# Optimization experiments

Measured on AMD Instinct MI355X. Metric: run time of the kernel, lower is better.

Reference implementation:

```python
import jax, jax.numpy as jnp
import numpy as np
import math

B, LA, LB, D, H = 8, 2048, 2048, 512, 512

def setup_inputs() -> dict:
    key = jax.random.key(0)
    ks = jax.random.split(key, 6)
    return {
        "input_a": jax.random.normal(ks[0], (B, LA, D), dtype=jnp.float32),
        "input_b": jax.random.normal(ks[1], (B, LB, D), dtype=jnp.float32),
        "mask_a": jax.random.randint(ks[2], (B, LA), 0, 2, dtype=jnp.int32),
        "mask_b": jax.random.randint(ks[3], (B, LB), 0, 2, dtype=jnp.int32),
        "Wa": jax.random.normal(ks[4], (D, H), dtype=jnp.float32) * (1.0 / math.sqrt(D)),
        "ba": jnp.zeros((H,), dtype=jnp.float32),
        "Wb": jax.random.normal(ks[5], (D, H), dtype=jnp.float32) * (1.0 / math.sqrt(D)),
        "bb": jnp.zeros((H,), dtype=jnp.float32),
    }

def reference(input_a, input_b, mask_a, mask_b, Wa, ba, Wb, bb):
    scale = 1.0 / math.sqrt(D)  # math.sqrt(input_dim_a)
    mapped_a = input_a @ Wa + ba            # [B, La, H]
    mapped_b = input_b @ Wb + bb            # [B, Lb, H]
    # final_mask = (mask_a outer mask_b) == 0
    final_mask = (mask_a[:, :, None] * mask_b[:, None, :]) == 0  # [B, La, Lb]
    scores = jnp.einsum('bih,bjh->bij', mapped_a, mapped_b) * scale
    scores = jnp.where(final_mask, jnp.float32(-1e9), scores)
    # attentions_a = softmax over Lb; attentions_b^T = softmax over La axis
    att_a = jax.nn.softmax(scores, axis=-1)   # [B, La, Lb]
    att_bT = jax.nn.softmax(scores, axis=1)   # [B, La, Lb] (= attentions_b.transpose(1,2))
    output_a = jnp.einsum('bij,bjd->bid', att_bT, input_b)  # [B, La, D]
    output_b = jnp.einsum('bij,bid->bjd', att_a, input_a)   # [B, Lb, D]
    return (output_a + input_a, output_b + input_b)
```

## Files before the change

### kernel.cpp

```cpp
#include <hip/hip_runtime.h>
#include <hip/hip_bf16.h>

#define BATCH 8
#define LSEQ 2048
#define DDIM 512

using f32x4 = __attribute__((ext_vector_type(4))) float;
using s16x8 = __attribute__((ext_vector_type(8))) short;
using s16x4 = __attribute__((ext_vector_type(4))) short;

static __device__ __forceinline__ unsigned short f2b(float f) {
  __hip_bfloat16 h = __float2bfloat16(f);
  return __builtin_bit_cast(unsigned short, h);
}
static __device__ __forceinline__ float b2f(unsigned short u) {
  unsigned int v = ((unsigned int)u) << 16;
  return __builtin_bit_cast(float, v);
}

static __device__ __forceinline__ void gld16(const unsigned short* g, unsigned short* l) {
  __builtin_amdgcn_global_load_lds(
      (__attribute__((address_space(1))) void*)(g),
      (__attribute__((address_space(3))) void*)(l), 16, 0, 0);
}

__device__ __forceinline__ void mfma_kloop(
    const unsigned short* __restrict__ A, const unsigned short* __restrict__ Bt,
    int K, int lda, int ldb, unsigned short* sA, unsigned short* sB,
    int tid, f32x4 acc[4][4]) {
  const int wave = tid >> 6, lane = tid & 63;
  const int wm = (wave >> 1) * 64, wn = (wave & 1) * 64;
  const int lr = lane & 15, lq = lane >> 4;
  const int srow = tid >> 2;
  const int sk = (tid & 3) * 8;
  unsigned short* dA0 = sA + wave * 512;
  unsigned short* dA1 = sA + 2048 + wave * 512;
  unsigned short* dB0 = sB + wave * 512;
  unsigned short* dB1 = sB + 2048 + wave * 512;
  const unsigned short* pa0 = A + (size_t)srow * lda + sk;
  const unsigned short* pa1 = A + (size_t)(srow + 64) * lda + sk;
  const unsigned short* pb0 = Bt + (size_t)srow * ldb + sk;
  const unsigned short* pb1 = Bt + (size_t)(srow + 64) * ldb + sk;
  for (int k0 = 0; k0 < K; k0 += 32) {
    gld16(pa0 + k0, dA0);
    gld16(pa1 + k0, dA1);
    gld16(pb0 + k0, dB0);
    gld16(pb1 + k0, dB1);
    __syncthreads();
    s16x8 af[4], bf[4];
#pragma unroll
    for (int r = 0; r < 4; ++r)
      af[r] = *(const s16x8*)(sA + (wm + r * 16 + lr) * 32 + lq * 8);
#pragma unroll
    for (int c = 0; c < 4; ++c)
      bf[c] = *(const s16x8*)(sB + (wn + c * 16 + lr) * 32 + lq * 8);
#pragma unroll
    for (int r = 0; r < 4; ++r)
#pragma unroll
      for (int c = 0; c < 4; ++c)
        acc[r][c] = __builtin_amdgcn_mfma_f32_16x16x32_bf16(af[r], bf[c], acc[r][c], 0, 0, 0);
    __syncthreads();
  }
}

__global__ __launch_bounds__(256) void k_prep(const float* __restrict__ in_a,
                                              const float* __restrict__ in_b,
                                              const int* __restrict__ ma,
                                              const int* __restrict__ mb,
                                              unsigned short* __restrict__ oa,
                                              unsigned short* __restrict__ ob,
                                              float* __restrict__ Pa,
                                              float* __restrict__ Pb) {
  int z = blockIdx.z;
  const float* in = z ? in_b : in_a;
  const int* mask = z ? mb : ma;
  unsigned short* o16 = z ? ob : oa;
  float* partial = z ? Pb : Pa;
  int b = blockIdx.y;
  int l0 = blockIdx.x * 32;
  __shared__ int sm[32];
  if (threadIdx.x < 32) sm[threadIdx.x] = mask[b * LSEQ + l0 + threadIdx.x];
  __syncthreads();
  int d = threadIdx.x * 2;
  const float* base = in + ((size_t)b * LSEQ + l0) * DDIM + d;
  unsigned short* obase = o16 + ((size_t)b * LSEQ + l0) * DDIM + d;
  float ax = 0.f, ay = 0.f;
#pragma unroll 4
  for (int r = 0; r < 32; ++r) {
    float2 v = *(const float2*)(base + (size_t)r * DDIM);
    ushort2 u; u.x = f2b(v.x); u.y = f2b(v.y);
    *(ushort2*)(obase + (size_t)r * DDIM) = u;
    if (sm[r] == 0) { ax += v.x; ay += v.y; }
  }
  float2 o; o.x = ax; o.y = ay;
  *(float2*)(partial + ((size_t)(b * 64 + blockIdx.x)) * DDIM + d) = o;
}

__global__ __launch_bounds__(256) void k_p2(const float* __restrict__ Pa,
                                            const float* __restrict__ Pb,
                                            float* __restrict__ Ca,
                                            float* __restrict__ Cb) {
  int g = blockIdx.x;
  const float* src = (g < 8) ? Pa : Pb;
  float* dst = (g < 8) ? Ca : Cb;
  int b = g & 7;
  int d = threadIdx.x * 2;
  float ax = 0.f, ay = 0.f;
  for (int c = 0; c < 64; ++c) {
    float2 v = *(const float2*)(src + ((size_t)(b * 64 + c)) * DDIM + d);
    ax += v.x; ay += v.y;
  }
  dst[b * DDIM + d] = ax * (1.0f / LSEQ);
  dst[b * DDIM + d + 1] = ay * (1.0f / LSEQ);
}

__global__ __launch_bounds__(256) void k_transposeW(const float* __restrict__ Wa,
                                                    const float* __restrict__ Wb,
                                                    unsigned short* __restrict__ WaT,
                                                    unsigned short* __restrict__ WbT) {
  int gidx = blockIdx.x * 256 + threadIdx.x;
  const float* W = (gidx < 512 * 512) ? Wa : Wb;
  unsigned short* WT = (gidx < 512 * 512) ? WaT : WbT;
  int idx = gidx & (512 * 512 - 1);
  int h = idx >> 9, d = idx & 511;
  WT[idx] = f2b(W[d * DDIM + h]);
}

__global__ __launch_bounds__(256) void k_gemm_bias(const unsigned short* __restrict__ a16,
                                                   const unsigned short* __restrict__ b16,
                                                   const unsigned short* __restrict__ WaT,
                                                   const unsigned short* __restrict__ WbT,
                                                   const float* __restrict__ ba,
                                                   const float* __restrict__ bb,
                                                   unsigned short* __restrict__ mapa,
                                                   unsigned short* __restrict__ mapb) {
  int id = blockIdx.x;
  int g = id >> 5, rem = id & 31;
  int bn = (rem >> 3) * 128;
  int f = g * 8 + (rem & 7);
  int bm = (f & 127) * 128;
  int z = f >> 7;
  const unsigned short* A = z ? b16 : a16;
  const unsigned short* Bt = z ? WbT : WaT;
  const float* bias = z ? bb : ba;
  unsigned short* Cout = z ? mapb : mapa;
  __shared__ __align__(16) unsigned short sA[128 * 32], sB[128 * 32];
  f32x4 acc[4][4];
  f32x4 zero = {0.f, 0.f, 0.f, 0.f};
#pragma unroll
  for (int r = 0; r < 4; ++r)
#pragma unroll
    for (int c = 0; c < 4; ++c) acc[r][c] = zero;
  mfma_kloop(A + (size_t)bm * DDIM, Bt + (size_t)bn * DDIM, DDIM, DDIM, DDIM,
             sA, sB, threadIdx.x, acc);
  int wave = threadIdx.x >> 6, lane = threadIdx.x & 63;
  int wm = (wave >> 1) * 64, wn = (wave & 1) * 64, lr = lane & 15, lq = lane >> 4;
#pragma unroll
  for (int r = 0; r < 4; ++r)
#pragma unroll
    for (int c = 0; c < 4; ++c)
#pragma unroll
      for (int rr = 0; rr < 4; ++rr) {
        int row = bm + wm + r * 16 + lq * 4 + rr;
        int col = bn + wn + c * 16 + lr;
        Cout[(size_t)row * DDIM + col] = f2b(acc[r][c][rr] + bias[col]);
      }
}

__global__ __launch_bounds__(256) void k_scores(const unsigned short* __restrict__ mapa,
                                                const unsigned short* __restrict__ mapb,
                                                const int* __restrict__ mask_a,
                                                const int* __restrict__ mask_b,
                                                unsigned short* __restrict__ E,
                                                unsigned short* __restrict__ Et,
                                                float* __restrict__ Zrow,
                                                float* __restrict__ Zcol) {
  int id = blockIdx.x;
  int low = id & 7, rest = id >> 3;
  int sub = rest & 15, Ghi = rest >> 4;
  int G = Ghi * 8 + low;
  int b = G >> 4, super = G & 15;
  int bi = (((super >> 2) << 2) + (sub >> 2)) * 128;
  int bj = (((super & 3) << 2) + (sub & 3)) * 128;
  __shared__ __align__(16) unsigned short smem[16384];
  __shared__ int sMa[128], sMb[128];
  int tid = threadIdx.x;
  if (tid < 128)
    sMa[tid] = mask_a[b * LSEQ + bi + tid];
  else
    sMb[tid - 128] = mask_b[b * LSEQ + bj + tid - 128];
  f32x4 acc[4][4];
  f32x4 zero = {0.f, 0.f, 0.f, 0.f};
#pragma unroll
  for (int r = 0; r < 4; ++r)
#pragma unroll
    for (int c = 0; c < 4; ++c) acc[r][c] = zero;
  mfma_kloop(mapa + ((size_t)b * LSEQ + bi) * DDIM, mapb + ((size_t)b * LSEQ + bj) * DDIM,
             DDIM, DDIM, DDIM, smem, smem + 4096, tid, acc);
  const float scale = 0.044194173824159216f;
  int wave = tid >> 6, lane = tid & 63;
  int wm = (wave >> 1) * 64, wn = (wave & 1) * 64, lr = lane & 15, lq = lane >> 4;
  unsigned short* Eb = E + (size_t)b * LSEQ * LSEQ + (size_t)bi * LSEQ + bj;
  float colp[4] = {0.f, 0.f, 0.f, 0.f};
  float rowp[4][4];
#pragma unroll
  for (int r = 0; r < 4; ++r) {
#pragma unroll
    for (int rr = 0; rr < 4; ++rr) rowp[r][rr] = 0.f;
#pragma unroll
    for (int c = 0; c < 4; ++c) {
      int jl = wn + c * 16 + lr;
      int mb_ = sMb[jl];
      s16x4 t;
#pragma unroll
      for (int rr = 0; rr < 4; ++rr) {
        int il = wm + r * 16 + lq * 4 + rr;
        float e = (sMa[il] && mb_) ? __expf(acc[r][c][rr] * scale) : 0.f;
        rowp[r][rr] += e;
        colp[c] += e;
        unsigned short eb = f2b(e);
        t[rr] = (short)eb;
        Eb[(size_t)il * LSEQ + jl] = eb;
      }
      int il0 = wm + r * 16 + lq * 4;
      *(s16x4*)(smem + jl * 128 + (il0 ^ ((jl & 7) << 4))) = t;
    }
  }
#pragma unroll
  for (int r = 0; r < 4; ++r)
#pragma unroll
    for (int rr = 0; rr < 4; ++rr) {
      float v = rowp[r][rr];
      v += __shfl_xor(v, 1);
      v += __shfl_xor(v, 2);
      v += __shfl_xor(v, 4);
      v += __shfl_xor(v, 8);
      if (lr == 0) {
        int il = wm + r * 16 + lq * 4 + rr;
        atomicAdd(&Zrow[b * LSEQ + bi + il], v);
      }
    }
#pragma unroll
  for (int c = 0; c < 4; ++c) {
    float v = colp[c];
    v += __shfl_xor(v, 16);
    v += __shfl_xor(v, 32);
    if (lq == 0) atomicAdd(&Zcol[b * LSEQ + bj + wn + c * 16 + lr], v);
  }
  __syncthreads();
  unsigned short* EtB = Et + (size_t)b * LSEQ * LSEQ + (size_t)bj * LSEQ + bi;
#pragma unroll
  for (int p = 0; p < 8; ++p) {
    int idx = p * 256 + tid;
    int jlr = idx >> 4, chk = idx & 15;
    s16x8 v = *(const s16x8*)(smem + jlr * 128 + ((chk * 8) ^ ((jlr & 7) << 4)));
    *(s16x8*)(EtB + (size_t)jlr * LSEQ + chk * 8) = v;
  }
}

__global__ __launch_bounds__(256) void k_scaleT(const unsigned short* __restrict__ a16,
                                                const unsigned short* __restrict__ b16,
                                                const float* __restrict__ Zrow,
                                                const float* __restrict__ Zcol,
                                                unsigned short* __restrict__ atS,
                                                unsigned short* __restrict__ btS) {
  int zz = blockIdx.z;
  int b = zz & 7, sel = zz >> 3;
  const unsigned short* in = sel ? b16 : a16;
  const float* Z = sel ? Zcol : Zrow;
  unsigned short* out = sel ? btS : atS;
  int i0 = blockIdx.y * 64, d0 = blockIdx.x * 64;
  __shared__ unsigned short lt[64 * 65];
  __shared__ float zinv[64];
  if (threadIdx.x < 64) {
    float z = Z[b * LSEQ + i0 + threadIdx.x];
    zinv[threadIdx.x] = (z > 0.f) ? 1.f / z : 0.f;
  }
  __syncthreads();
  const unsigned short* ib = in + ((size_t)b * LSEQ + i0) * DDIM + d0;
#pragma unroll
  for (int p = 0; p < 16; ++p) {
    int idx = p * 256 + threadIdx.x;
    int dl = idx & 63, il = idx >> 6;
    lt[dl * 65 + il] = f2b(b2f(ib[(size_t)il * DDIM + dl]) * zinv[il]);
  }
  __syncthreads();
  unsigned short* ob = out + ((size_t)b * DDIM + d0) * LSEQ + i0;
#pragma unroll
  for (int p = 0; p < 16; ++p) {
    int idx = p * 256 + threadIdx.x;
    int il = idx & 63, dl = idx >> 6;
    ob[(size_t)dl * LSEQ + il] = lt[dl * 65 + il];
  }
}

__global__ __launch_bounds__(512, 2) void k_gemm_outs(
    const unsigned short* __restrict__ E, const unsigned short* __restrict__ Et,
    const unsigned short* __restrict__ btS, const unsigned short* __restrict__ atS,
    const unsigned short* __restrict__ a16, const unsigned short* __restrict__ b16,
    const float* __restrict__ Ca, const float* __restrict__ Cb,
    float* __restrict__ OutA, float* __restrict__ OutB) {
  int w = (blockIdx.x & 7) * 32 + (blockIdx.x >> 3);
  int mode = w >> 7;
  int r0 = w & 127;
  int b = r0 >> 4, tile = r0 & 15;
  int bm = (tile >> 1) * 256, bn = (tile & 1) * 256;
  const unsigned short* Aop = (mode ? Et : E) + (size_t)b * LSEQ * LSEQ + (size_t)bm * LSEQ;
  const unsigned short* Bop = (mode ? atS : btS) + (size_t)b * DDIM * LSEQ + (size_t)bn * LSEQ;
  const unsigned short* addin = mode ? b16 : a16;
  const float* Cvec = mode ? Ca : Cb;
  float* Out = mode ? OutB : OutA;

  __shared__ __align__(16) unsigned short sA[4 * 8192], sB[4 * 8192];
  const int tid = threadIdx.x;
  const int wave = tid >> 6, lane = tid & 63;
  const int wr = wave >> 2, wc = wave & 3;
  const int lr = lane & 15, lq = lane >> 4;

  const int srow = tid >> 2;
  const int kcsw = ((tid & 3) ^ (srow & 3)) * 8;
  const unsigned short* pa0 = Aop + (size_t)srow * LSEQ + kcsw;
  const unsigned short* pa1 = pa0 + (size_t)128 * LSEQ;
  const unsigned short* pb0 = Bop + (size_t)srow * LSEQ + kcsw;
  const unsigned short* pb1 = pb0 + (size_t)128 * LSEQ;
  unsigned short* dA = sA + wave * 512;
  unsigned short* dB = sB + wave * 512;

  int aoff[8], boff[4];
#pragma unroll
  for (int m = 0; m < 8; ++m)
    aoff[m] = (wr * 128 + m * 16 + lr) * 32 + (lq ^ (lr & 3)) * 8;
#pragma unroll
  for (int n = 0; n < 4; ++n)
    boff[n] = (wc * 64 + n * 16 + lr) * 32 + (lq ^ (lr & 3)) * 8;

  f32x4 acc[8][4];
  f32x4 zero = {0.f, 0.f, 0.f, 0.f};
#pragma unroll
  for (int m = 0; m < 8; ++m)
#pragma unroll
    for (int n = 0; n < 4; ++n) acc[m][n] = zero;

#define SGA(c) { const int sl_ = ((c) & 3) * 8192; \
  gld16(pa0 + (size_t)(c) * 32, dA + sl_); \
  gld16(pa1 + (size_t)(c) * 32, dA + sl_ + 4096); }
#define SGB(c) { const int sl_ = ((c) & 3) * 8192; \
  gld16(pb0 + (size_t)(c) * 32, dB + sl_); \
  gld16(pb1 + (size_t)(c) * 32, dB + sl_ + 4096); }

  SGA(0); SGB(0); SGA(1); SGB(1); SGA(2); SGB(2);
  asm volatile("s_waitcnt vmcnt(8)\ns_barrier" ::: "memory");

  for (int j = 0; j < 64; ++j) {
    const int sl = (j & 3) * 8192;
    s16x8 af[8];
#pragma unroll
    for (int m = 0; m < 8; ++m) af[m] = *(const s16x8*)(sA + sl + aoff[m]);
    s16x8 bf0 = *(const s16x8*)(sB + sl + boff[0]);
    s16x8 bf1 = *(const s16x8*)(sB + sl + boff[1]);
    if (j < 61) SGA(j + 3);
    __builtin_amdgcn_s_setprio(1);
#pragma unroll
    for (int m = 0; m < 8; ++m) {
      acc[m][0] = __builtin_amdgcn_mfma_f32_16x16x32_bf16(af[m], bf0, acc[m][0], 0, 0, 0);
      acc[m][1] = __builtin_amdgcn_mfma_f32_16x16x32_bf16(af[m], bf1, acc[m][1], 0, 0, 0);
    }
    __builtin_amdgcn_s_setprio(0);
    asm volatile("s_barrier" ::: "memory");
    s16x8 bf2 = *(const s16x8*)(sB + sl + boff[2]);
    s16x8 bf3 = *(const s16x8*)(sB + sl + boff[3]);
    if (j < 61) SGB(j + 3);
    __builtin_amdgcn_s_setprio(1);
#pragma unroll
    for (int m = 0; m < 8; ++m) {
      acc[m][2] = __builtin_amdgcn_mfma_f32_16x16x32_bf16(af[m], bf2, acc[m][2], 0, 0, 0);
      acc[m][3] = __builtin_amdgcn_mfma_f32_16x16x32_bf16(af[m], bf3, acc[m][3], 0, 0, 0);
    }
    __builtin_amdgcn_s_setprio(0);
    if (j < 61)
      asm volatile("s_waitcnt vmcnt(8)\ns_barrier" ::: "memory");
    else if (j == 61)
      asm volatile("s_waitcnt vmcnt(4)\ns_barrier" ::: "memory");
    else
      asm volatile("s_waitcnt vmcnt(0)\ns_barrier" ::: "memory");
  }
#undef SGA
#undef SGB

#pragma unroll
  for (int m = 0; m < 8; ++m)
#pragma unroll
    for (int n = 0; n < 4; ++n)
#pragma unroll
      for (int rr = 0; rr < 4; ++rr) {
        int row = bm + wr * 128 + m * 16 + lq * 4 + rr;
        int col = bn + wc * 64 + n * 16 + lr;
        size_t o = ((size_t)b * LSEQ + row) * DDIM + col;
        Out[o] = acc[m][n][rr] + b2f(addin[o]) + Cvec[b * DDIM + col];
      }
}

extern "C" void kernel_launch(void* const* d_in, const int* in_sizes, int n_in,
                              void* d_out, int out_size, void* d_ws, size_t ws_size,
                              hipStream_t stream) {
  (void)in_sizes; (void)n_in; (void)out_size; (void)ws_size;
  const float* in_a = (const float*)d_in[0];
  const float* in_b = (const float*)d_in[1];
  const int* ma = (const int*)d_in[2];
  const int* mb = (const int*)d_in[3];
  const float* Wa = (const float*)d_in[4];
  const float* ba = (const float*)d_in[5];
  const float* Wb = (const float*)d_in[6];
  const float* bb = (const float*)d_in[7];
  float* out = (float*)d_out;

  char* ws = (char*)d_ws;
  const size_t MB = 1ull << 20;
  unsigned short* a16 = (unsigned short*)(ws + 0 * MB);
  unsigned short* b16 = (unsigned short*)(ws + 16 * MB);
  unsigned short* WaT = (unsigned short*)(ws + 32 * MB);
  unsigned short* WbT = (unsigned short*)(ws + 32 * MB + 512 * 1024);
  unsigned short* mapa = (unsigned short*)(ws + 33 * MB);
  unsigned short* mapb = (unsigned short*)(ws + 49 * MB);
  unsigned short* E = (unsigned short*)(ws + 65 * MB);
  unsigned short* atS = (unsigned short*)(ws + 129 * MB);
  unsigned short* btS = (unsigned short*)(ws + 145 * MB);
  float* Zrow = (float*)(ws + 161 * MB);
  float* Zcol = (float*)(ws + 161 * MB + 65536);
  float* Ca = (float*)(ws + 161 * MB + 2 * 65536);
  float* Cb = (float*)(ws + 161 * MB + 2 * 65536 + 16384);
  float* Pa = (float*)(ws + 162 * MB);
  float* Pb = (float*)(ws + 163 * MB);
  unsigned short* Et = (unsigned short*)(ws + 164 * MB);

  hipMemsetAsync(Zrow, 0, 2 * 65536, stream);
  k_prep<<<dim3(64, 8, 2), 256, 0, stream>>>(in_a, in_b, ma, mb, a16, b16, Pa, Pb);
  k_transposeW<<<2048, 256, 0, stream>>>(Wa, Wb, WaT, WbT);
  k_p2<<<16, 256, 0, stream>>>(Pa, Pb, Ca, Cb);
  k_gemm_bias<<<1024, 256, 0, stream>>>(a16, b16, WaT, WbT, ba, bb, mapa, mapb);
  k_scores<<<2048, 256, 0, stream>>>(mapa, mapb, ma, mb, E, Et, Zrow, Zcol);
  k_scaleT<<<dim3(8, 32, 16), 256, 0, stream>>>(a16, b16, Zrow, Zcol, atS, btS);
  k_gemm_outs<<<256, 512, 0, stream>>>(E, Et, btS, atS, a16, b16, Ca, Cb,
                                       out, out + (size_t)BATCH * LSEQ * DDIM);
}
```

Measured before the change: 324.7 us.

## Enlarge score tiles to 256x256 with pipelined 4-stage direct-to-LDS loads

Rewrites the scores GEMM kernel to use 256x256 output tiles with 512 threads (8 waves) instead of 128x128 with 256 threads. The new version uses a custom 4-slot ring of global_load_lds prefetches with manual vmcnt waits, splits the B fragment loads between two MFMA phases, and raises wave priority around the MFMA blocks. Larger tiles cut redundant operand loads and quarter the number of blocks. In exchange it uses 128KB of LDS and 128 accumulator registers per lane, which limits occupancy, and 512 blocks may leave the CUs less evenly loaded.

```diff
diff --git a/kernel.cpp b/kernel.cpp
--- a/kernel.cpp
+++ b/kernel.cpp
@@ -167,93 +167,158 @@
       }
 }
 
-__global__ __launch_bounds__(256) void k_scores(const unsigned short* __restrict__ mapa,
-                                                const unsigned short* __restrict__ mapb,
-                                                const int* __restrict__ mask_a,
-                                                const int* __restrict__ mask_b,
-                                                unsigned short* __restrict__ E,
-                                                unsigned short* __restrict__ Et,
-                                                float* __restrict__ Zrow,
-                                                float* __restrict__ Zcol) {
-  int id = blockIdx.x;
-  int low = id & 7, rest = id >> 3;
-  int sub = rest & 15, Ghi = rest >> 4;
-  int G = Ghi * 8 + low;
-  int b = G >> 4, super = G & 15;
-  int bi = (((super >> 2) << 2) + (sub >> 2)) * 128;
-  int bj = (((super & 3) << 2) + (sub & 3)) * 128;
-  __shared__ __align__(16) unsigned short smem[16384];
-  __shared__ int sMa[128], sMb[128];
-  int tid = threadIdx.x;
-  if (tid < 128)
+__global__ __launch_bounds__(512, 2) void k_scores(
+    const unsigned short* __restrict__ mapa, const unsigned short* __restrict__ mapb,
+    const int* __restrict__ mask_a, const int* __restrict__ mask_b,
+    unsigned short* __restrict__ E, unsigned short* __restrict__ Et,
+    float* __restrict__ Zrow, float* __restrict__ Zcol) {
+  int w = (blockIdx.x & 7) * 64 + (blockIdx.x >> 3);
+  int b = w >> 6, t = w & 63;
+  int bi = (t >> 3) * 256, bj = (t & 7) * 256;
+  const unsigned short* Aop = mapa + ((size_t)b * LSEQ + bi) * DDIM;
+  const unsigned short* Bop = mapb + ((size_t)b * LSEQ + bj) * DDIM;
+
+  __shared__ __align__(16) unsigned short smem[65536];
+  unsigned short* sA = smem;
+  unsigned short* sB = smem + 32768;
+  __shared__ int sMa[256], sMb[256];
+
+  const int tid = threadIdx.x;
+  const int wave = tid >> 6, lane = tid & 63;
+  const int wr = wave >> 2, wc = wave & 3;
+  const int lr = lane & 15, lq = lane >> 4;
+
+  const int srow = tid >> 2;
+  const int kcsw = ((tid & 3) ^ (srow & 3)) * 8;
+  const unsigned short* pa0 = Aop + (size_t)srow * DDIM + kcsw;
+  const unsigned short* pa1 = pa0 + (size_t)128 * DDIM;
+  const unsigned short* pb0 = Bop + (size_t)srow * DDIM + kcsw;
+  const unsigned short* pb1 = pb0 + (size_t)128 * DDIM;
+  unsigned short* dA = sA + wave * 512;
+  unsigned short* dB = sB + wave * 512;
+
+  int aoff[8], boff[4];
+#pragma unroll
+  for (int m = 0; m < 8; ++m)
+    aoff[m] = (wr * 128 + m * 16 + lr) * 32 + (lq ^ (lr & 3)) * 8;
+#pragma unroll
+  for (int n = 0; n < 4; ++n)
+    boff[n] = (wc * 64 + n * 16 + lr) * 32 + (lq ^ (lr & 3)) * 8;
+
+  f32x4 acc[8][4];
+  f32x4 zero = {0.f, 0.f, 0.f, 0.f};
+#pragma unroll
+  for (int m = 0; m < 8; ++m)
+#pragma unroll
+    for (int n = 0; n < 4; ++n) acc[m][n] = zero;
+
+#define SGA(c) { const int sl_ = ((c) & 3) * 8192; \
+  gld16(pa0 + (size_t)(c) * 32, dA + sl_); \
+  gld16(pa1 + (size_t)(c) * 32, dA + sl_ + 4096); }
+#define SGB(c) { const int sl_ = ((c) & 3) * 8192; \
+  gld16(pb0 + (size_t)(c) * 32, dB + sl_); \
+  gld16(pb1 + (size_t)(c) * 32, dB + sl_ + 4096); }
+
+  SGA(0); SGB(0); SGA(1); SGB(1); SGA(2); SGB(2);
+  asm volatile("s_waitcnt vmcnt(8)\ns_barrier" ::: "memory");
+
+  for (int j = 0; j < 16; ++j) {
+    const int sl = (j & 3) * 8192;
+    s16x8 af[8];
+#pragma unroll
+    for (int m = 0; m < 8; ++m) af[m] = *(const s16x8*)(sA + sl + aoff[m]);
+    s16x8 bf0 = *(const s16x8*)(sB + sl + boff[0]);
+    s16x8 bf1 = *(const s16x8*)(sB + sl + boff[1]);
+    if (j < 13) SGA(j + 3);
+    __builtin_amdgcn_s_setprio(1);
+#pragma unroll
+    for (int m = 0; m < 8; ++m) {
+      acc[m][0] = __builtin_amdgcn_mfma_f32_16x16x32_bf16(af[m], bf0, acc[m][0], 0, 0, 0);
+      acc[m][1] = __builtin_amdgcn_mfma_f32_16x16x32_bf16(af[m], bf1, acc[m][1], 0, 0, 0);
+    }
+    __builtin_amdgcn_s_setprio(0);
+    asm volatile("s_barrier" ::: "memory");
+    s16x8 bf2 = *(const s16x8*)(sB + sl + boff[2]);
+    s16x8 bf3 = *(const s16x8*)(sB + sl + boff[3]);
+    if (j < 13) SGB(j + 3);
+    __builtin_amdgcn_s_setprio(1);
+#pragma unroll
+    for (int m = 0; m < 8; ++m) {
+      acc[m][2] = __builtin_amdgcn_mfma_f32_16x16x32_bf16(af[m], bf2, acc[m][2], 0, 0, 0);
+      acc[m][3] = __builtin_amdgcn_mfma_f32_16x16x32_bf16(af[m], bf3, acc[m][3], 0, 0, 0);
+    }
+    __builtin_amdgcn_s_setprio(0);
+    if (j < 13)
+      asm volatile("s_waitcnt vmcnt(8)\ns_barrier" ::: "memory");
+    else if (j == 13)
+      asm volatile("s_waitcnt vmcnt(4)\ns_barrier" ::: "memory");
+    else
+      asm volatile("s_waitcnt vmcnt(0)\ns_barrier" ::: "memory");
+  }
+#undef SGA
+#undef SGB
+
+  if (tid < 256)
     sMa[tid] = mask_a[b * LSEQ + bi + tid];
   else
-    sMb[tid - 128] = mask_b[b * LSEQ + bj + tid - 128];
-  f32x4 acc[4][4];
-  f32x4 zero = {0.f, 0.f, 0.f, 0.f};
-#pragma unroll
-  for (int r = 0; r < 4; ++r)
-#pragma unroll
-    for (int c = 0; c < 4; ++c) acc[r][c] = zero;
-  mfma_kloop(mapa + ((size_t)b * LSEQ + bi) * DDIM, mapb + ((size_t)b * LSEQ + bj) * DDIM,
-             DDIM, DDIM, DDIM, smem, smem + 4096, tid, acc);
+    sMb[tid - 256] = mask_b[b * LSEQ + bj + tid - 256];
+  __syncthreads();
+
   const float scale = 0.044194173824159216f;
-  int wave = tid >> 6, lane = tid & 63;
-  int wm = (wave >> 1) * 64, wn = (wave & 1) * 64, lr = lane & 15, lq = lane >> 4;
   unsigned short* Eb = E + (size_t)b * LSEQ * LSEQ + (size_t)bi * LSEQ + bj;
+  float rowp[8][4];
   float colp[4] = {0.f, 0.f, 0.f, 0.f};
-  float rowp[4][4];
-#pragma unroll
-  for (int r = 0; r < 4; ++r) {
-#pragma unroll
-    for (int rr = 0; rr < 4; ++rr) rowp[r][rr] = 0.f;
-#pragma unroll
-    for (int c = 0; c < 4; ++c) {
-      int jl = wn + c * 16 + lr;
+#pragma unroll
+  for (int m = 0; m < 8; ++m) {
+#pragma unroll
+    for (int rr = 0; rr < 4; ++rr) rowp[m][rr] = 0.f;
+#pragma unroll
+    for (int n = 0; n < 4; ++n) {
+      int jl = wc * 64 + n * 16 + lr;
       int mb_ = sMb[jl];
-      s16x4 t;
+      s16x4 tq;
 #pragma unroll
       for (int rr = 0; rr < 4; ++rr) {
-        int il = wm + r * 16 + lq * 4 + rr;
-        float e = (sMa[il] && mb_) ? __expf(acc[r][c][rr] * scale) : 0.f;
-        rowp[r][rr] += e;
-        colp[c] += e;
+        int il = wr * 128 + m * 16 + lq * 4 + rr;
+        float e = (sMa[il] && mb_) ? __expf(acc[m][n][rr] * scale) : 0.f;
+        rowp[m][rr] += e;
+        colp[n] += e;
         unsigned short eb = f2b(e);
-        t[rr] = (short)eb;
+        tq[rr] = (short)eb;
         Eb[(size_t)il * LSEQ + jl] = eb;
       }
-      int il0 = wm + r * 16 + lq * 4;
-      *(s16x4*)(smem + jl * 128 + (il0 ^ ((jl & 7) << 4))) = t;
+      int il0 = wr * 128 + m * 16 + lq * 4;
+      *(s16x4*)(smem + jl * 256 + (il0 ^ ((jl & 7) << 3))) = tq;
     }
   }
 #pragma unroll
-  for (int r = 0; r < 4; ++r)
+  for (int m = 0; m < 8; ++m)
 #pragma unroll
     for (int rr = 0; rr < 4; ++rr) {
-      float v = rowp[r][rr];
+      float v = rowp[m][rr];
       v += __shfl_xor(v, 1);
       v += __shfl_xor(v, 2);
       v += __shfl_xor(v, 4);
       v += __shfl_xor(v, 8);
       if (lr == 0) {
-        int il = wm + r * 16 + lq * 4 + rr;
+        int il = wr * 128 + m * 16 + lq * 4 + rr;
         atomicAdd(&Zrow[b * LSEQ + bi + il], v);
       }
     }
 #pragma unroll
-  for (int c = 0; c < 4; ++c) {
-    float v = colp[c];
+  for (int n = 0; n < 4; ++n) {
+    float v = colp[n];
     v += __shfl_xor(v, 16);
     v += __shfl_xor(v, 32);
-    if (lq == 0) atomicAdd(&Zcol[b * LSEQ + bj + wn + c * 16 + lr], v);
+    if (lq == 0) atomicAdd(&Zcol[b * LSEQ + bj + wc * 64 + n * 16 + lr], v);
   }
   __syncthreads();
   unsigned short* EtB = Et + (size_t)b * LSEQ * LSEQ + (size_t)bj * LSEQ + bi;
 #pragma unroll
-  for (int p = 0; p < 8; ++p) {
-    int idx = p * 256 + tid;
-    int jlr = idx >> 4, chk = idx & 15;
-    s16x8 v = *(const s16x8*)(smem + jlr * 128 + ((chk * 8) ^ ((jlr & 7) << 4)));
+  for (int p = 0; p < 16; ++p) {
+    int idx = p * 512 + tid;
+    int jlr = idx >> 5, chk = idx & 31;
+    s16x8 v = *(const s16x8*)(smem + jlr * 256 + ((chk * 8) ^ ((jlr & 7) << 3)));
     *(s16x8*)(EtB + (size_t)jlr * LSEQ + chk * 8) = v;
   }
 }
@@ -438,7 +503,7 @@
   k_transposeW<<<2048, 256, 0, stream>>>(Wa, Wb, WaT, WbT);
   k_p2<<<16, 256, 0, stream>>>(Pa, Pb, Ca, Cb);
   k_gemm_bias<<<1024, 256, 0, stream>>>(a16, b16, WaT, WbT, ba, bb, mapa, mapb);
-  k_scores<<<2048, 256, 0, stream>>>(mapa, mapb, ma, mb, E, Et, Zrow, Zcol);
+  k_scores<<<512, 512, 0, stream>>>(mapa, mapb, ma, mb, E, Et, Zrow, Zcol);
   k_scaleT<<<dim3(8, 32, 16), 256, 0, stream>>>(a16, b16, Zrow, Zcol, atS, btS);
   k_gemm_outs<<<256, 512, 0, stream>>>(E, Et, btS, atS, a16, b16, Ca, Cb,
                                        out, out + (size_t)BATCH * LSEQ * DDIM);
```

Result: no change. 330.4 us (+1.8%).
